# Performance work log

Measured on AMD Instinct MI355X. Metric: run time of the kernel, lower is better.

## Reference

```python
import jax, jax.numpy as jnp
import numpy as np

HEADS = 8
DIM_HEAD = 64
SCALE = DIM_HEAD ** -0.5


def setup_inputs() -> dict:
    key = jax.random.key(0)
    ks = jax.random.split(key, 6)
    b, n, d = 2, 4096, 1024
    inner = HEADS * DIM_HEAD  # 512
    x = jax.random.normal(ks[0], (b, n, d), dtype=jnp.float32)
    Wq = jax.random.normal(ks[1], (d, inner), dtype=jnp.float32) * (d ** -0.5)
    Wk = jax.random.normal(ks[2], (d, inner), dtype=jnp.float32) * (d ** -0.5)
    Wv = jax.random.normal(ks[3], (d, inner), dtype=jnp.float32) * (d ** -0.5)
    Wout = jax.random.normal(ks[4], (inner, d), dtype=jnp.float32) * (inner ** -0.5)
    bout = jnp.zeros((d,), dtype=jnp.float32)
    return {"x": x, "Wq": Wq, "Wk": Wk, "Wv": Wv, "Wout": Wout, "bout": bout}


def reference(x, Wq, Wk, Wv, Wout, bout):
    b, n, _ = x.shape
    h, dh = HEADS, DIM_HEAD
    # self-attention: context = x
    q = (x @ Wq).reshape(b, n, h, dh).transpose(0, 2, 1, 3)  # b h n d
    k = (x @ Wk).reshape(b, n, h, dh).transpose(0, 2, 1, 3)
    v = (x @ Wv).reshape(b, n, h, dh).transpose(0, 2, 1, 3)
    sim = jnp.einsum('bhid,bhjd->bhij', q, k) * SCALE  # full score matrix
    attn = jax.nn.softmax(sim, axis=-1)
    out = jnp.einsum('bhij,bhjd->bhid', attn, v)
    out = out.transpose(0, 2, 1, 3).reshape(b, n, h * dh)  # b n (h d)
    return out @ Wout + bout
```

## Files before the change

### kernel.cpp

```cpp
#include <hip/hip_runtime.h>
#include <hip/hip_bf16.h>

typedef __bf16 bf16x8 __attribute__((ext_vector_type(8)));
typedef __bf16 bf16x4 __attribute__((ext_vector_type(4)));
typedef float floatx4 __attribute__((ext_vector_type(4)));

#define MFMA16(a, b, c) __builtin_amdgcn_mfma_f32_16x16x32_bf16((a), (b), (c), 0, 0, 0)

__device__ __forceinline__ void stage16(const __bf16* g, __bf16* lds_base) {
  __builtin_amdgcn_global_load_lds(
      (__attribute__((address_space(1))) void*)(void*)g,
      (__attribute__((address_space(3))) void*)lds_base, 16, 0, 0);
}

__global__ void detect_dtype(const unsigned int* __restrict__ x, int* __restrict__ flag) {
  __shared__ int cnt;
  if (threadIdx.x == 0) cnt = 0;
  __syncthreads();
  int c = 0;
  for (int i = threadIdx.x; i < 4096; i += 256) {
    const unsigned f = (x[i] >> 7) & 0xFF;
    c += (f >= 100 && f <= 140) ? 1 : 0;
  }
  atomicAdd(&cnt, c);
  __syncthreads();
  if (threadIdx.x == 0) *flag = (cnt > 2048) ? 1 : 0;
}

__global__ __launch_bounds__(256) void transpose3_conv(
    const void* __restrict__ s0, const void* __restrict__ s1,
    const void* __restrict__ s2, __bf16* __restrict__ dst,
    int R, int C, const int* __restrict__ flagp) {
  __shared__ __bf16 t[32][33];
  const int isbf = *flagp;
  const void* src = (blockIdx.z == 0) ? s0 : (blockIdx.z == 1) ? s1 : s2;
  __bf16* d = dst + (size_t)blockIdx.z * R * C;
  const int bx = blockIdx.x * 32, by = blockIdx.y * 32;
  const int x = threadIdx.x & 31, y0 = threadIdx.x >> 5;
#pragma unroll
  for (int i = y0; i < 32; i += 8) {
    const size_t idx = (size_t)(by + i) * C + bx + x;
    t[i][x] = isbf ? ((const __bf16*)src)[idx] : (__bf16)(((const float*)src)[idx]);
  }
  __syncthreads();
#pragma unroll
  for (int i = y0; i < 32; i += 8) d[(size_t)(bx + i) * R + by + x] = t[x][i];
}

__global__ __launch_bounds__(256) void transpose_conv(const void* __restrict__ src,
                                                      __bf16* __restrict__ dst,
                                                      int R, int C,
                                                      const int* __restrict__ flagp) {
  __shared__ __bf16 t[32][33];
  const int isbf = *flagp;
  const int bx = blockIdx.x * 32, by = blockIdx.y * 32;
  const int x = threadIdx.x & 31, y0 = threadIdx.x >> 5;
#pragma unroll
  for (int i = y0; i < 32; i += 8) {
    const size_t idx = (size_t)(by + i) * C + bx + x;
    t[i][x] = isbf ? ((const __bf16*)src)[idx] : (__bf16)(((const float*)src)[idx]);
  }
  __syncthreads();
#pragma unroll
  for (int i = y0; i < 32; i += 8) dst[(size_t)(bx + i) * R + by + x] = t[x][i];
}

__global__ __launch_bounds__(256) void vp_transpose(const __bf16* __restrict__ V,
                                                    __bf16* __restrict__ VP) {
  alignas(16) __shared__ __bf16 t[64][64];
  const int bh = blockIdx.y, s0 = blockIdx.x * 64;
  const int row = threadIdx.x >> 2, part = threadIdx.x & 3;
  const __bf16* src = V + (size_t)bh * 262144 + (size_t)(s0 + row) * 64 + part * 16;
  *(bf16x8*)&t[row][part * 16] = *(const bf16x8*)src;
  *(bf16x8*)&t[row][part * 16 + 8] = *(const bf16x8*)(src + 8);
  __syncthreads();
  const int d = row, og = part;
  bf16x8 w0, w1;
#pragma unroll
  for (int e = 0; e < 8; e++) {
    const int o0 = og * 16 + e, o1 = og * 16 + 8 + e;
    w0[e] = t[(o0 & 3) * 16 + (o0 >> 2)][d];
    w1[e] = t[(o1 & 3) * 16 + (o1 >> 2)][d];
  }
  __bf16* dst = VP + (size_t)bh * 262144 + (size_t)d * 4096 + s0 + og * 16;
  *(bf16x8*)dst = w0;
  *(bf16x8*)(dst + 8) = w1;
}

template <int A_DUAL>
__global__ __launch_bounds__(256) void gemm_bt(
    const void* __restrict__ Araw, const __bf16* __restrict__ Bt,
    void* __restrict__ Cv, void* __restrict__ Cv2, int M, int N, int K,
    const void* __restrict__ bias, int permute, int egress_dual,
    size_t zsB, size_t zsC, const int* __restrict__ flagp) {
  alignas(16) __shared__ __bf16 As[128 * 32];
  alignas(16) __shared__ __bf16 Bs[128 * 32];
  const int isbf = *flagp;
  Bt += blockIdx.z * zsB;
  const size_t zoff = (size_t)blockIdx.z * zsC;
  const int tid = threadIdx.x;
  const int wave = tid >> 6, lane = tid & 63;
  const int m0 = blockIdx.y * 128, n0 = blockIdx.x * 128;
  const int wm = (wave & 1) * 64, wn = (wave >> 1) * 64;
  const int fr = lane & 15, fq = lane >> 4;

  const floatx4 zero4 = {0.f, 0.f, 0.f, 0.f};
  floatx4 acc[4][4];
#pragma unroll
  for (int i = 0; i < 4; i++)
#pragma unroll
    for (int j = 0; j < 4; j++) acc[i][j] = zero4;

  const int lrow = lane >> 2;
  const int lk = (lane & 3) * 8;

  for (int k0 = 0; k0 < K; k0 += 32) {
#pragma unroll
    for (int cc = 0; cc < 2; ++cc) {
      const int c = 2 * wave + cc;
      const size_t aoff = (size_t)(m0 + c * 16 + lrow) * K + k0 + lk;
      if (A_DUAL && !isbf) {
        const float* p = (const float*)Araw + aoff;
        const float4 f0 = *(const float4*)p;
        const float4 f1 = *(const float4*)(p + 4);
        bf16x8 v;
        v[0] = (__bf16)f0.x; v[1] = (__bf16)f0.y; v[2] = (__bf16)f0.z; v[3] = (__bf16)f0.w;
        v[4] = (__bf16)f1.x; v[5] = (__bf16)f1.y; v[6] = (__bf16)f1.z; v[7] = (__bf16)f1.w;
        *(bf16x8*)&As[c * 512 + lane * 8] = v;
      } else {
        stage16((const __bf16*)Araw + aoff, &As[c * 512]);
      }
      stage16(Bt + (size_t)(n0 + c * 16 + lrow) * K + k0 + lk, &Bs[c * 512]);
    }
    __syncthreads();
    bf16x8 af[4], bg[4];
#pragma unroll
    for (int mt = 0; mt < 4; mt++)
      af[mt] = *(const bf16x8*)&As[(wm + mt * 16 + fr) * 32 + fq * 8];
#pragma unroll
    for (int nt = 0; nt < 4; nt++)
      bg[nt] = *(const bf16x8*)&Bs[(wn + nt * 16 + fr) * 32 + fq * 8];
#pragma unroll
    for (int mt = 0; mt < 4; mt++)
#pragma unroll
      for (int nt = 0; nt < 4; nt++)
        acc[mt][nt] = MFMA16(af[mt], bg[nt], acc[mt][nt]);
    __syncthreads();
  }

  const float qs = (permute && blockIdx.z == 0) ? 0.18033688011112042f
                                                : 1.0f;
#pragma unroll
  for (int mt = 0; mt < 4; mt++)
#pragma unroll
    for (int nt = 0; nt < 4; nt++)
#pragma unroll
      for (int r = 0; r < 4; r++) {
        const int row = m0 + wm + mt * 16 + fq * 4 + r;
        const int col = n0 + wn + nt * 16 + fr;
        float v = acc[mt][nt][r] * qs;
        if (bias)
          v += isbf ? (float)((const __bf16*)bias)[col] : ((const float*)bias)[col];
        if (permute) {
          const int bh = (row >> 12) * 8 + (col >> 6);
          const int s = row & 4095, d = col & 63;
          const size_t pidx = (size_t)bh * 262144 + (size_t)s * 64 + d;
          if (blockIdx.z == 2)
            ((__bf16*)Cv2)[pidx] = (__bf16)v;
          else
            ((__bf16*)Cv)[zoff + pidx] = (__bf16)v;
        } else {
          const size_t idx = (size_t)row * N + col;
          if (egress_dual && !isbf)
            ((float*)Cv)[idx] = v;
          else
            ((__bf16*)Cv)[idx] = (__bf16)v;
        }
      }
}

#define ATT_S 4096
#define KV_SPLIT 2
__global__ __launch_bounds__(256) void attn_flash(
    const __bf16* __restrict__ Qa, const __bf16* __restrict__ Ka,
    const __bf16* __restrict__ VPa, float* __restrict__ Of,
    float* __restrict__ lp) {
  alignas(16) __shared__ __bf16 Kl[2][64 * 64];
  alignas(16) __shared__ __bf16 Vl[2][64 * 64];
  alignas(16) __shared__ __bf16 Pl[4 * 32 * 64];
  const int tid = threadIdx.x, wave = tid >> 6, lane = tid & 63;
  const int bh = blockIdx.y, b = bh >> 3, h = bh & 7;
  const int z = blockIdx.z;
  const int q0 = blockIdx.x * 128 + wave * 32;
  const int fr = lane & 15, fq = lane >> 4;
  const __bf16* Qb = Qa + (size_t)bh * ATT_S * 64;
  const __bf16* Kb = Ka + (size_t)bh * ATT_S * 64;
  const __bf16* Vb = VPa + (size_t)bh * ATT_S * 64;

  const int sw0 = ((fq ^ (fr & 7)) * 8);
  const int sw1 = (((fq + 4) ^ (fr & 7)) * 8);
  const int r0 = tid >> 3;
  const int ssw = (((tid & 7) ^ (r0 & 7)) * 8);

  bf16x8 aq[2][2];
#pragma unroll
  for (int mt = 0; mt < 2; mt++)
#pragma unroll
    for (int kt = 0; kt < 2; kt++)
      aq[mt][kt] = *(const bf16x8*)(Qb + (size_t)(q0 + mt * 16 + fr) * 64 + kt * 32 + fq * 8);

  const floatx4 zero4 = {0.f, 0.f, 0.f, 0.f};
  floatx4 o[2][4];
  float lsum[2][4];
#pragma unroll
  for (int mt = 0; mt < 2; mt++) {
#pragma unroll
    for (int nt = 0; nt < 4; nt++) o[mt][nt] = zero4;
#pragma unroll
    for (int r = 0; r < 4; r++) lsum[mt][r] = 0.f;
  }

  const int JT = (ATT_S / 64) / KV_SPLIT;
  const int jbase = z * JT;

#pragma unroll
  for (int c = 0; c < 2; c++) {
    stage16(Kb + (size_t)(jbase * 64 + c * 32 + r0) * 64 + ssw,
            &Kl[0][(c * 256 + wave * 64) * 8]);
    stage16(Vb + (size_t)(c * 32 + r0) * 4096 + jbase * 64 + ssw,
            &Vl[0][(c * 256 + wave * 64) * 8]);
  }

  for (int j = 0; j < JT; ++j) {
    __syncthreads();
    const int cur = j & 1;
    if (j + 1 < JT) {
      const int kv1 = (jbase + j + 1) * 64;
#pragma unroll
      for (int c = 0; c < 2; c++) {
        stage16(Kb + (size_t)(kv1 + c * 32 + r0) * 64 + ssw,
                &Kl[1 - cur][(c * 256 + wave * 64) * 8]);
        stage16(Vb + (size_t)(c * 32 + r0) * 4096 + kv1 + ssw,
                &Vl[1 - cur][(c * 256 + wave * 64) * 8]);
      }
    }
    const __bf16* Klc = Kl[cur];
    const __bf16* Vlc = Vl[cur];

    floatx4 s4[2][4];
#pragma unroll
    for (int nt = 0; nt < 4; nt++) {
      bf16x8 bk0 = *(const bf16x8*)&Klc[(nt * 16 + fr) * 64 + sw0];
      bf16x8 bk1 = *(const bf16x8*)&Klc[(nt * 16 + fr) * 64 + sw1];
#pragma unroll
      for (int mt = 0; mt < 2; mt++) {
        floatx4 zz = zero4;
        zz = MFMA16(aq[mt][0], bk0, zz);
        zz = MFMA16(aq[mt][1], bk1, zz);
        s4[mt][nt] = zz;
      }
    }

#pragma unroll
    for (int mt = 0; mt < 2; mt++)
#pragma unroll
      for (int r = 0; r < 4; r++) {
        bf16x4 pv;
        float psum = 0.f;
#pragma unroll
        for (int nt = 0; nt < 4; nt++) {
          const float p = __builtin_amdgcn_exp2f(s4[mt][nt][r]);
          pv[nt] = (__bf16)p;
          psum += p;
        }
        lsum[mt][r] += psum;
        const int row = wave * 32 + mt * 16 + fq * 4 + r;
        const int vg = (fr >> 1) ^ ((fq * 4 + r) & 7);
        *(bf16x4*)&Pl[row * 64 + vg * 8 + (fr & 1) * 4] = pv;
      }
    asm volatile("s_waitcnt lgkmcnt(0)" ::: "memory");

    bf16x8 bv[4][2];
#pragma unroll
    for (int nt = 0; nt < 4; nt++) {
      bv[nt][0] = *(const bf16x8*)&Vlc[(nt * 16 + fr) * 64 + sw0];
      bv[nt][1] = *(const bf16x8*)&Vlc[(nt * 16 + fr) * 64 + sw1];
    }
#pragma unroll
    for (int mt = 0; mt < 2; mt++) {
      const int prow = (wave * 32 + mt * 16 + fr) * 64;
      bf16x8 ap0 = *(const bf16x8*)&Pl[prow + sw0];
      bf16x8 ap1 = *(const bf16x8*)&Pl[prow + sw1];
#pragma unroll
      for (int nt = 0; nt < 4; nt++) {
        o[mt][nt] = MFMA16(ap0, bv[nt][0], o[mt][nt]);
        o[mt][nt] = MFMA16(ap1, bv[nt][1], o[mt][nt]);
      }
    }
  }

#pragma unroll
  for (int off = 1; off < 16; off <<= 1)
#pragma unroll
    for (int mt = 0; mt < 2; mt++)
#pragma unroll
      for (int r = 0; r < 4; r++) lsum[mt][r] += __shfl_xor(lsum[mt][r], off, 64);

  float* Ofz = Of + (size_t)z * 8192 * 512;
  float* lz = lp + (size_t)z * 16 * 4096;
#pragma unroll
  for (int mt = 0; mt < 2; mt++)
#pragma unroll
    for (int r = 0; r < 4; r++) {
      const int row = q0 + mt * 16 + fq * 4 + r;
      if (fr == 0) lz[bh * 4096 + row] = lsum[mt][r];
#pragma unroll
      for (int nt = 0; nt < 4; nt++) {
        const int col = h * 64 + nt * 16 + fr;
        Ofz[(size_t)(b * ATT_S + row) * 512 + col] = o[mt][nt][r];
      }
    }
}

__global__ __launch_bounds__(256) void attn_combine(
    const float* __restrict__ Of, const float* __restrict__ lp,
    __bf16* __restrict__ O) {
  const size_t i = ((size_t)blockIdx.x * 256 + threadIdx.x) * 8;
  const int row = (int)(i >> 9), colb = (int)(i & 511);
  const int bh = (row >> 12) * 8 + (colb >> 6), qrow = row & 4095;
  const float l = lp[bh * 4096 + qrow] + lp[16 * 4096 + bh * 4096 + qrow];
  const float inv = 1.0f / l;
  const float4 a0 = *(const float4*)(Of + i);
  const float4 a1 = *(const float4*)(Of + i + 4);
  const float4 b0 = *(const float4*)(Of + 8192 * 512 + i);
  const float4 b1 = *(const float4*)(Of + 8192 * 512 + i + 4);
  bf16x8 w;
  w[0] = (__bf16)((a0.x + b0.x) * inv); w[1] = (__bf16)((a0.y + b0.y) * inv);
  w[2] = (__bf16)((a0.z + b0.z) * inv); w[3] = (__bf16)((a0.w + b0.w) * inv);
  w[4] = (__bf16)((a1.x + b1.x) * inv); w[5] = (__bf16)((a1.y + b1.y) * inv);
  w[6] = (__bf16)((a1.z + b1.z) * inv); w[7] = (__bf16)((a1.w + b1.w) * inv);
  *(bf16x8*)(O + i) = w;
}

extern "C" void kernel_launch(void* const* d_in, const int* in_sizes, int n_in,
                              void* d_out, int out_size, void* d_ws, size_t ws_size,
                              hipStream_t stream) {
  (void)in_sizes; (void)n_in; (void)out_size; (void)ws_size;
  const void* x = d_in[0];
  const void* Wq = d_in[1];
  const void* Wk = d_in[2];
  const void* Wv = d_in[3];
  const void* Wout = d_in[4];
  const void* bout = d_in[5];

  char* ws = (char*)d_ws;
  int* flag = (int*)ws;
  __bf16* wtq = (__bf16*)(ws + (1u << 20));
  __bf16* wto = (__bf16*)(ws + (4u << 20));
  __bf16* Q = (__bf16*)(ws + (5u << 20));
  __bf16* K = (__bf16*)(ws + (13u << 20));
  __bf16* VP = (__bf16*)(ws + (21u << 20));
  __bf16* O = (__bf16*)(ws + (29u << 20));
  __bf16* Vtmp = O;
  float* Of = (float*)(ws + (38u << 20));
  float* lp = (float*)(ws + (72u << 20));

  detect_dtype<<<1, 256, 0, stream>>>((const unsigned int*)x, flag);

  transpose3_conv<<<dim3(16, 32, 3), 256, 0, stream>>>(Wq, Wk, Wv, wtq, 1024, 512, flag);
  transpose_conv<<<dim3(32, 16), 256, 0, stream>>>(Wout, wto, 512, 1024, flag);

  gemm_bt<1><<<dim3(4, 64, 3), 256, 0, stream>>>(
      x, wtq, Q, Vtmp, 8192, 512, 1024, nullptr, 1, 0,
      (size_t)512 * 1024, (size_t)8192 * 512, flag);

  vp_transpose<<<dim3(64, 16), 256, 0, stream>>>(Vtmp, VP);

  attn_flash<<<dim3(32, 16, KV_SPLIT), 256, 0, stream>>>(Q, K, VP, Of, lp);

  attn_combine<<<2048, 256, 0, stream>>>(Of, lp, O);

  gemm_bt<0><<<dim3(8, 64, 1), 256, 0, stream>>>(
      O, wto, d_out, nullptr, 8192, 1024, 512, bout, 0, 1, 0, 0, flag);
}
```

Measured before the change: 291.3 us.

## Compute softmax row sums via MFMA with ones and merge weight transposes

The attention kernel now computes row sums by multiplying the P fragments by a vector of ones with extra MFMAs, replacing the per-element adds and the final cross-lane shuffle reduction. The P staging buffer is halved by processing one 16-row tile at a time, which interleaves exp and LDS writes with the PV MFMAs. The four weight transposes are also merged into one launch, with out-of-range blocks exiting early. The costs are two extra MFMAs per tile, an extra LDS wait for each tile, and row sums taken from bf16-rounded probabilities.

```diff
diff --git a/kernel.cpp b/kernel.cpp
--- a/kernel.cpp
+++ b/kernel.cpp
@@ -27,14 +27,18 @@
   if (threadIdx.x == 0) *flag = (cnt > 2048) ? 1 : 0;
 }
 
-__global__ __launch_bounds__(256) void transpose3_conv(
+__global__ __launch_bounds__(256) void transpose4_conv(
     const void* __restrict__ s0, const void* __restrict__ s1,
-    const void* __restrict__ s2, __bf16* __restrict__ dst,
-    int R, int C, const int* __restrict__ flagp) {
+    const void* __restrict__ s2, const void* __restrict__ s3,
+    __bf16* __restrict__ wtq, __bf16* __restrict__ wto,
+    const int* __restrict__ flagp) {
   __shared__ __bf16 t[32][33];
+  const int z = blockIdx.z;
+  const int R = (z == 3) ? 512 : 1024, C = (z == 3) ? 1024 : 512;
+  if (blockIdx.x * 32 >= C || blockIdx.y * 32 >= R) return;
   const int isbf = *flagp;
-  const void* src = (blockIdx.z == 0) ? s0 : (blockIdx.z == 1) ? s1 : s2;
-  __bf16* d = dst + (size_t)blockIdx.z * R * C;
+  const void* src = (z == 0) ? s0 : (z == 1) ? s1 : (z == 2) ? s2 : s3;
+  __bf16* d = (z == 3) ? wto : wtq + (size_t)z * 512 * 1024;
   const int bx = blockIdx.x * 32, by = blockIdx.y * 32;
   const int x = threadIdx.x & 31, y0 = threadIdx.x >> 5;
 #pragma unroll
@@ -45,24 +49,6 @@
   __syncthreads();
 #pragma unroll
   for (int i = y0; i < 32; i += 8) d[(size_t)(bx + i) * R + by + x] = t[x][i];
-}
-
-__global__ __launch_bounds__(256) void transpose_conv(const void* __restrict__ src,
-                                                      __bf16* __restrict__ dst,
-                                                      int R, int C,
-                                                      const int* __restrict__ flagp) {
-  __shared__ __bf16 t[32][33];
-  const int isbf = *flagp;
-  const int bx = blockIdx.x * 32, by = blockIdx.y * 32;
-  const int x = threadIdx.x & 31, y0 = threadIdx.x >> 5;
-#pragma unroll
-  for (int i = y0; i < 32; i += 8) {
-    const size_t idx = (size_t)(by + i) * C + bx + x;
-    t[i][x] = isbf ? ((const __bf16*)src)[idx] : (__bf16)(((const float*)src)[idx]);
-  }
-  __syncthreads();
-#pragma unroll
-  for (int i = y0; i < 32; i += 8) dst[(size_t)(bx + i) * R + by + x] = t[x][i];
 }
 
 __global__ __launch_bounds__(256) void vp_transpose(const __bf16* __restrict__ V,
@@ -187,7 +173,7 @@
     float* __restrict__ lp) {
   alignas(16) __shared__ __bf16 Kl[2][64 * 64];
   alignas(16) __shared__ __bf16 Vl[2][64 * 64];
-  alignas(16) __shared__ __bf16 Pl[4 * 32 * 64];
+  alignas(16) __shared__ __bf16 Pl[4 * 16 * 64];
   const int tid = threadIdx.x, wave = tid >> 6, lane = tid & 63;
   const int bh = blockIdx.y, b = bh >> 3, h = bh & 7;
   const int z = blockIdx.z;
@@ -209,15 +195,18 @@
     for (int kt = 0; kt < 2; kt++)
       aq[mt][kt] = *(const bf16x8*)(Qb + (size_t)(q0 + mt * 16 + fr) * 64 + kt * 32 + fq * 8);
 
+  bf16x8 vones;
+#pragma unroll
+  for (int e = 0; e < 8; e++) vones[e] = (__bf16)1.0f;
+
   const floatx4 zero4 = {0.f, 0.f, 0.f, 0.f};
   floatx4 o[2][4];
-  float lsum[2][4];
+  floatx4 lacc[2];
 #pragma unroll
   for (int mt = 0; mt < 2; mt++) {
 #pragma unroll
     for (int nt = 0; nt < 4; nt++) o[mt][nt] = zero4;
-#pragma unroll
-    for (int r = 0; r < 4; r++) lsum[mt][r] = 0.f;
+    lacc[mt] = zero4;
   }
 
   const int JT = (ATT_S / 64) / KV_SPLIT;
@@ -261,34 +250,29 @@
       }
     }
 
-#pragma unroll
-    for (int mt = 0; mt < 2; mt++)
-#pragma unroll
-      for (int r = 0; r < 4; r++) {
-        bf16x4 pv;
-        float psum = 0.f;
-#pragma unroll
-        for (int nt = 0; nt < 4; nt++) {
-          const float p = __builtin_amdgcn_exp2f(s4[mt][nt][r]);
-          pv[nt] = (__bf16)p;
-          psum += p;
-        }
-        lsum[mt][r] += psum;
-        const int row = wave * 32 + mt * 16 + fq * 4 + r;
-        const int vg = (fr >> 1) ^ ((fq * 4 + r) & 7);
-        *(bf16x4*)&Pl[row * 64 + vg * 8 + (fr & 1) * 4] = pv;
-      }
-    asm volatile("s_waitcnt lgkmcnt(0)" ::: "memory");
-
     bf16x8 bv[4][2];
 #pragma unroll
     for (int nt = 0; nt < 4; nt++) {
       bv[nt][0] = *(const bf16x8*)&Vlc[(nt * 16 + fr) * 64 + sw0];
       bv[nt][1] = *(const bf16x8*)&Vlc[(nt * 16 + fr) * 64 + sw1];
     }
+
 #pragma unroll
     for (int mt = 0; mt < 2; mt++) {
-      const int prow = (wave * 32 + mt * 16 + fr) * 64;
+      if (mt == 1)
+        asm volatile("s_waitcnt lgkmcnt(0)" ::: "memory");
+#pragma unroll
+      for (int r = 0; r < 4; r++) {
+        bf16x4 pv;
+#pragma unroll
+        for (int nt = 0; nt < 4; nt++)
+          pv[nt] = (__bf16)__builtin_amdgcn_exp2f(s4[mt][nt][r]);
+        const int row = fq * 4 + r;
+        const int vg = (fr >> 1) ^ (row & 7);
+        *(bf16x4*)&Pl[(wave * 16 + row) * 64 + vg * 8 + (fr & 1) * 4] = pv;
+      }
+      asm volatile("s_waitcnt lgkmcnt(0)" ::: "memory");
+      const int prow = (wave * 16 + fr) * 64;
       bf16x8 ap0 = *(const bf16x8*)&Pl[prow + sw0];
       bf16x8 ap1 = *(const bf16x8*)&Pl[prow + sw1];
 #pragma unroll
@@ -296,15 +280,10 @@
         o[mt][nt] = MFMA16(ap0, bv[nt][0], o[mt][nt]);
         o[mt][nt] = MFMA16(ap1, bv[nt][1], o[mt][nt]);
       }
-    }
-  }
-
-#pragma unroll
-  for (int off = 1; off < 16; off <<= 1)
-#pragma unroll
-    for (int mt = 0; mt < 2; mt++)
-#pragma unroll
-      for (int r = 0; r < 4; r++) lsum[mt][r] += __shfl_xor(lsum[mt][r], off, 64);
+      lacc[mt] = MFMA16(ap0, vones, lacc[mt]);
+      lacc[mt] = MFMA16(ap1, vones, lacc[mt]);
+    }
+  }
 
   float* Ofz = Of + (size_t)z * 8192 * 512;
   float* lz = lp + (size_t)z * 16 * 4096;
@@ -313,7 +292,7 @@
 #pragma unroll
     for (int r = 0; r < 4; r++) {
       const int row = q0 + mt * 16 + fq * 4 + r;
-      if (fr == 0) lz[bh * 4096 + row] = lsum[mt][r];
+      if (fr == 0) lz[bh * 4096 + row] = lacc[mt][r];
 #pragma unroll
       for (int nt = 0; nt < 4; nt++) {
         const int col = h * 64 + nt * 16 + fr;
@@ -367,8 +346,8 @@
 
   detect_dtype<<<1, 256, 0, stream>>>((const unsigned int*)x, flag);
 
-  transpose3_conv<<<dim3(16, 32, 3), 256, 0, stream>>>(Wq, Wk, Wv, wtq, 1024, 512, flag);
-  transpose_conv<<<dim3(32, 16), 256, 0, stream>>>(Wout, wto, 512, 1024, flag);
+  transpose4_conv<<<dim3(32, 32, 4), 256, 0, stream>>>(Wq, Wk, Wv, Wout,
+                                                       wtq, wto, flag);
 
   gemm_bt<1><<<dim3(4, 64, 3), 256, 0, stream>>>(
       x, wtq, Q, Vtmp, 8192, 512, 1024, nullptr, 1, 0,
```

Result: slower. 305.0 us (+4.7%).
